# Optimization experiments

Measured on AMD Instinct MI355X. Metric: run time of the kernel, lower is better.

## Reference

```python
import jax, jax.numpy as jnp
import numpy as np

BETA = 0.95
NUM_STEPS = 32


def setup_inputs() -> dict:
    key = jax.random.key(0)
    ks = jax.random.split(key, 6)
    B, IN, D, P = 1024, 512, 256, 8
    total = D * P
    x = jax.random.normal(ks[0], (B, IN), jnp.float32)
    W_proj = jax.random.normal(ks[1], (IN, total), jnp.float32) / np.sqrt(IN)
    b_proj = jnp.zeros((total,), jnp.float32)
    # uniform threshold distribution, sorted: linspace(0.5, 2.0, P)
    thresholds = jnp.linspace(0.5, 2.0, P, dtype=jnp.float32)
    rate_W = jax.random.normal(ks[2], (P, 1), jnp.float32) / np.sqrt(P)
    rate_b = jnp.zeros((1,), jnp.float32)
    conv1_w = jax.random.normal(ks[3], (P // 2, P, 3), jnp.float32) / np.sqrt(P * 3)
    conv1_b = jnp.zeros((P // 2,), jnp.float32)
    conv2_w = jax.random.normal(ks[4], (1, P // 2, 1), jnp.float32) / np.sqrt(P // 2)
    conv2_b = jnp.zeros((1,), jnp.float32)
    fusion = jnp.array([0.6, 0.4], jnp.float32)
    return dict(x=x, W_proj=W_proj, b_proj=b_proj, thresholds=thresholds,
                rate_W=rate_W, rate_b=rate_b, conv1_w=conv1_w, conv1_b=conv1_b,
                conv2_w=conv2_w, conv2_b=conv2_b, fusion=fusion)


def _conv1d(x, w, b):
    # x: [N, C_in, T], w: [C_out, C_in, K] -> [N, C_out, T] (SAME padding)
    y = jax.lax.conv_general_dilated(x, w, window_strides=(1,), padding='SAME',
                                     dimension_numbers=('NCH', 'OIH', 'NCH'))
    return y + b[None, :, None]


def reference(x, W_proj, b_proj, thresholds, rate_W, rate_b,
              conv1_w, conv1_b, conv2_w, conv2_b, fusion):
    B = x.shape[0]
    P = thresholds.shape[0]
    D = W_proj.shape[1] // P
    # constant input current per neuron: [B, D, P]
    I = (x @ W_proj + b_proj).reshape(B, D, P)

    # LIF recurrence (snntorch Leaky, reset_mechanism='subtract'):
    #   reset = H(mem_prev - thr); mem = beta*mem_prev + I - reset*thr; spk = H(mem - thr)
    def step(mem, _):
        reset = (mem > thresholds).astype(mem.dtype)
        mem = BETA * mem + I - reset * thresholds
        spk = (mem > thresholds).astype(mem.dtype)
        return mem, spk

    mem0 = jnp.zeros((B, D, P), x.dtype)
    _, spikes = jax.lax.scan(step, mem0, None, length=NUM_STEPS)  # [T, B, D, P]

    # rate branch
    rates = spikes.mean(axis=0)                        # [B, D, P]
    rate_dec = (rates @ rate_W)[..., 0] + rate_b[0]    # [B, D]

    # temporal branch: [B*D, P, T]
    s = jnp.transpose(spikes, (1, 2, 3, 0)).reshape(B * D, P, NUM_STEPS)
    h = jax.nn.relu(_conv1d(s, conv1_w, conv1_b))
    h = _conv1d(h, conv2_w, conv2_b)                   # [B*D, 1, T]
    temp_dec = h.mean(axis=-1).reshape(B, D)

    fw = jax.nn.softmax(fusion)
    return fw[0] * rate_dec + fw[1] * temp_dec
```

## Files before the change

kernel.cpp:

```cpp
#include <hip/hip_runtime.h>


constexpr int IN_DIM  = 512;
constexpr int D_DIM   = 256;
constexpr int NTOT    = 2048;
constexpr int T_STEPS = 32;

typedef _Float16 f16x8 __attribute__((ext_vector_type(8)));
typedef float    f32x4 __attribute__((ext_vector_type(4)));
typedef ushort   ushort8 __attribute__((ext_vector_type(8)));

#define GLOBAL_AS __attribute__((address_space(1)))
#define LDS_AS    __attribute__((address_space(3)))

__device__ __forceinline__ void split_f16(float v, ushort& h, ushort& l) {
    const _Float16 hf = (_Float16)v;
    const _Float16 lf = (_Float16)((v - (float)hf) * 2048.0f);
    h = __builtin_bit_cast(ushort, hf);
    l = __builtin_bit_cast(ushort, lf);
}

__global__ __launch_bounds__(256)
void popcode_prep(const float* __restrict__ x, const float* __restrict__ Wp,
                  ushort* __restrict__ Ah, ushort* __restrict__ Al,
                  ushort* __restrict__ Bh, ushort* __restrict__ Bl)
{
    __shared__ float tile[64][69];
    const int t = threadIdx.x;
    if (blockIdx.x < 256) {
        const int idx = (blockIdx.x * 256 + t) * 8;
        float v[8];
        *reinterpret_cast<float4*>(v)     = *reinterpret_cast<const float4*>(x + idx);
        *reinterpret_cast<float4*>(v + 4) = *reinterpret_cast<const float4*>(x + idx + 4);
        __align__(16) ushort h[8], l[8];
#pragma unroll
        for (int j = 0; j < 8; ++j) split_f16(v[j], h[j], l[j]);
        *reinterpret_cast<ushort8*>(Ah + idx) = *reinterpret_cast<const ushort8*>(h);
        *reinterpret_cast<ushort8*>(Al + idx) = *reinterpret_cast<const ushort8*>(l);
    } else {
        const int ib = blockIdx.x - 256;
        const int k0 = (ib >> 5) * 64;
        const int c0 = (ib & 31) * 64;
        {
            const int r = t >> 2, cq = (t & 3) * 16;
#pragma unroll
            for (int j = 0; j < 4; ++j)
                *reinterpret_cast<float4*>(&tile[r][cq + j * 4]) =
                    *reinterpret_cast<const float4*>(Wp + (size_t)(k0 + r) * NTOT + c0 + cq + j * 4);
        }
        __syncthreads();
        const int rr = t >> 2, kc2 = (t & 3) * 16;
        __align__(16) ushort h[16], l[16];
#pragma unroll
        for (int j = 0; j < 16; ++j) split_f16(tile[kc2 + j][rr], h[j], l[j]);
        ushort* dh = Bh + (size_t)(c0 + rr) * 512 + k0 + kc2;
        ushort* dl = Bl + (size_t)(c0 + rr) * 512 + k0 + kc2;
        *reinterpret_cast<ushort8*>(dh)     = *reinterpret_cast<const ushort8*>(h);
        *reinterpret_cast<ushort8*>(dh + 8) = *reinterpret_cast<const ushort8*>(h + 8);
        *reinterpret_cast<ushort8*>(dl)     = *reinterpret_cast<const ushort8*>(l);
        *reinterpret_cast<ushort8*>(dl + 8) = *reinterpret_cast<const ushort8*>(l + 8);
    }
}

__global__ __launch_bounds__(256, 2)
void popcode_fused(const ushort* __restrict__ Ah_g, const ushort* __restrict__ Al_g,
                   const ushort* __restrict__ Bh_g, const ushort* __restrict__ Bl_g,
                   const float* __restrict__ bp,
                   const float* __restrict__ thrs,
                   const float* __restrict__ rateW,
                   const float* __restrict__ rateB,
                   const float* __restrict__ c1w,
                   const float* __restrict__ c1b,
                   const float* __restrict__ c2w,
                   const float* __restrict__ c2b,
                   const float* __restrict__ fus,
                   float* __restrict__ out)
{
    __shared__ __align__(16) ushort Lds[2][4][64][32];
    __shared__ float Itile[64][65];
    __shared__ float lut[3][2][16][4];
    __shared__ float wlds[96];

    const int tid  = threadIdx.x;
    const int w    = tid >> 6;
    const int lane = tid & 63;

    const int wg = (blockIdx.x & 7) * 64 + (blockIdx.x >> 3);
    const int b0 = (wg & 15) * 64;
    const int c0 = (wg >> 4) * 64;

    const ushort* gbase = (w == 0) ? Ah_g : (w == 1) ? Al_g : (w == 2) ? Bh_g : Bl_g;
    const int     t0    = (w < 2) ? b0 : c0;
    const int     srow  = lane >> 2;
    const int     schk  = (lane & 3) * 8;

    const int wr = (w >> 1) * 32;
    const int wc = (w & 1) * 32;
    const int lr = lane & 15;
    const int lg = lane >> 4;

    const f32x4 zero = {0.f, 0.f, 0.f, 0.f};
    f32x4 acch[2][2] = {{zero, zero}, {zero, zero}};
    f32x4 accl[2][2] = {{zero, zero}, {zero, zero}};

    LDS_AS char* lds0 = (LDS_AS char*)&Lds[0][0][0][0];

    auto stage = [&](int buf, int kt) {
        const int koff = kt * 32 + schk;
#pragma unroll
        for (int i = 0; i < 4; ++i) {
            const ushort* src = gbase + (size_t)(t0 + srow + 16 * i) * 512 + koff;
            const int loff = __builtin_amdgcn_readfirstlane(buf * 16384 + w * 4096 + i * 1024);
            __builtin_amdgcn_global_load_lds((const GLOBAL_AS uint*)src,
                                             (LDS_AS uint*)(lds0 + loff), 16, 0, 0);
        }
    };

    auto compute = [&](int buf) {
        f16x8 ah[2], al[2], bh[2], bl[2];
#pragma unroll
        for (int m = 0; m < 2; ++m) {
            const int row = wr + m * 16 + lr;
            ah[m] = *(const f16x8*)&Lds[buf][0][row][lg * 8];
            al[m] = *(const f16x8*)&Lds[buf][1][row][lg * 8];
        }
#pragma unroll
        for (int n = 0; n < 2; ++n) {
            const int col = wc + n * 16 + lr;
            bh[n] = *(const f16x8*)&Lds[buf][2][col][lg * 8];
            bl[n] = *(const f16x8*)&Lds[buf][3][col][lg * 8];
        }
#pragma unroll
        for (int m = 0; m < 2; ++m)
#pragma unroll
            for (int n = 0; n < 2; ++n) {
                acch[m][n] = __builtin_amdgcn_mfma_f32_16x16x32_f16(ah[m], bh[n], acch[m][n], 0, 0, 0);
                accl[m][n] = __builtin_amdgcn_mfma_f32_16x16x32_f16(al[m], bh[n], accl[m][n], 0, 0, 0);
                accl[m][n] = __builtin_amdgcn_mfma_f32_16x16x32_f16(ah[m], bl[n], accl[m][n], 0, 0, 0);
            }
    };

    if (tid < 96) wlds[tid] = c1w[tid];
    stage(0, 0);
    __syncthreads();

    for (int e = tid; e < 384; e += 256) {
        const int k  = e >> 7;
        const int j  = (e >> 6) & 1;
        const int nb = (e >> 2) & 15;
        const int c  = e & 3;
        float v = (k == 1 && j == 0) ? c1b[c] : 0.f;
#pragma unroll
        for (int p = 0; p < 4; ++p)
            v = fmaf((float)((nb >> p) & 1), wlds[(c * 8 + j * 4 + p) * 3 + k], v);
        (&lut[0][0][0][0])[e] = v;
    }

    for (int kt = 0; kt < 16; ++kt) {
        if (kt < 15) stage((kt + 1) & 1, kt + 1);
        compute(kt & 1);
        __syncthreads();
    }

    const float s = 1.0f / 2048.0f;
#pragma unroll
    for (int m = 0; m < 2; ++m)
#pragma unroll
        for (int n = 0; n < 2; ++n)
#pragma unroll
            for (int v = 0; v < 4; ++v)
                Itile[wr + m * 16 + lg * 4 + v][wc + n * 16 + lr] =
                    acch[m][n][v] + accl[m][n][v] * s;
    __syncthreads();

    float w2c[4];
#pragma unroll
    for (int c = 0; c < 4; ++c) w2c[c] = c2w[c];
    float rW[8], thrv[8];
#pragma unroll
    for (int p = 0; p < 8; ++p) { rW[p] = rateW[p]; thrv[p] = thrs[p]; }
    const float rb_ = rateB[0];
    const float bb2 = c2b[0];
    const float f0 = fus[0], f1 = fus[1];
    const float fm = fmaxf(f0, f1);
    const float e0 = __expf(f0 - fm), e1 = __expf(f1 - fm);
    const float inv = 1.f / (e0 + e1);
    const float fw0 = e0 * inv, fw1 = e1 * inv;

    const float* lutf = &lut[0][0][0][0];

    for (int half = 0; half < 2; ++half) {
        const int nb   = tid + half * 256;
        const int row  = nb >> 3;
        const int dloc = nb & 7;
        const int dg   = (c0 >> 3) + dloc;

        const float* ip = &Itile[row][dloc * 8];
        const float4 bv0 = *reinterpret_cast<const float4*>(bp + dg * 8);
        const float4 bv1 = *reinterpret_cast<const float4*>(bp + dg * 8 + 4);
        const float bpx[8] = {bv0.x, bv0.y, bv0.z, bv0.w, bv1.x, bv1.y, bv1.z, bv1.w};

        float Iv[8], Imt[8], mem[8];
        bool  spk[8];
#pragma unroll
        for (int p = 0; p < 8; ++p) {
            Iv[p]  = ip[p] + bpx[p];
            Imt[p] = Iv[p] - thrv[p];
            mem[p] = 0.f;
            spk[p] = false;
        }

        unsigned nibL[4] = {0u, 0u, 0u, 0u}, nibH[4] = {0u, 0u, 0u, 0u};
#pragma unroll
        for (int t = 0; t < T_STEPS; ++t) {
            unsigned bl_ = 0u, bh_ = 0u;
#pragma unroll
            for (int p = 0; p < 8; ++p) {
                mem[p] = 0.95f * mem[p] + (spk[p] ? Imt[p] : Iv[p]);
                spk[p] = mem[p] > thrv[p];
            }
#pragma unroll
            for (int p = 0; p < 4; ++p) bl_ |= spk[p] ? (1u << p) : 0u;
#pragma unroll
            for (int p = 4; p < 8; ++p) bh_ |= spk[p] ? (1u << (p - 4)) : 0u;
            nibL[t >> 3] |= bl_ << (4 * (t & 7));
            nibH[t >> 3] |= bh_ << (4 * (t & 7));
        }

        float rsum = 0.f;
#pragma unroll
        for (int p = 0; p < 4; ++p) {
            const unsigned m = 0x11111111u << p;
            const int cL = __popc(nibL[0] & m) + __popc(nibL[1] & m)
                         + __popc(nibL[2] & m) + __popc(nibL[3] & m);
            const int cH = __popc(nibH[0] & m) + __popc(nibH[1] & m)
                         + __popc(nibH[2] & m) + __popc(nibH[3] & m);
            rsum = fmaf((float)cL, rW[p], rsum);
            rsum = fmaf((float)cH, rW[4 + p], rsum);
        }

        auto getn = [](const unsigned* a, int t) -> unsigned {
            return (a[t >> 3] >> (4 * (t & 7))) & 15u;
        };
        float tacc = 0.f;
        unsigned nlp = 0u, nhp = 0u;
        unsigned nlc = getn(nibL, 0), nhc = getn(nibH, 0);
#pragma unroll
        for (int t = 0; t < T_STEPS; ++t) {
            const unsigned nln = (t < 31) ? getn(nibL, t + 1) : 0u;
            const unsigned nhn = (t < 31) ? getn(nibH, t + 1) : 0u;
            const float4 a0 = *reinterpret_cast<const float4*>(lutf + (nlp     ) * 4);
            const float4 a1 = *reinterpret_cast<const float4*>(lutf + (nhp + 16) * 4);
            const float4 b0 = *reinterpret_cast<const float4*>(lutf + (nlc + 32) * 4);
            const float4 b1 = *reinterpret_cast<const float4*>(lutf + (nhc + 48) * 4);
            const float4 c0v = *reinterpret_cast<const float4*>(lutf + (nln + 64) * 4);
            const float4 c1v = *reinterpret_cast<const float4*>(lutf + (nhn + 80) * 4);
            const float h0_ = ((a0.x + a1.x) + (b0.x + b1.x)) + (c0v.x + c1v.x);
            const float h1_ = ((a0.y + a1.y) + (b0.y + b1.y)) + (c0v.y + c1v.y);
            const float h2_ = ((a0.z + a1.z) + (b0.z + b1.z)) + (c0v.z + c1v.z);
            const float h3_ = ((a0.w + a1.w) + (b0.w + b1.w)) + (c0v.w + c1v.w);
            tacc = fmaf(fmaxf(h0_, 0.f), w2c[0], tacc);
            tacc = fmaf(fmaxf(h1_, 0.f), w2c[1], tacc);
            tacc = fmaf(fmaxf(h2_, 0.f), w2c[2], tacc);
            tacc = fmaf(fmaxf(h3_, 0.f), w2c[3], tacc);
            nlp = nlc; nhp = nhc; nlc = nln; nhc = nhn;
        }

        const float rdec = rsum * (1.f / 32.f) + rb_;
        const float temp = tacc * (1.f / 32.f) + bb2;
        out[(b0 + row) * D_DIM + dg] = fw0 * rdec + fw1 * temp;
    }
}

extern "C" void kernel_launch(void* const* d_in, const int* in_sizes, int n_in,
                              void* d_out, int out_size, void* d_ws, size_t ws_size,
                              hipStream_t stream) {
    const float* x     = (const float*)d_in[0];
    const float* Wp    = (const float*)d_in[1];
    const float* bp    = (const float*)d_in[2];
    const float* thrs  = (const float*)d_in[3];
    const float* rateW = (const float*)d_in[4];
    const float* rateB = (const float*)d_in[5];
    const float* c1w   = (const float*)d_in[6];
    const float* c1b   = (const float*)d_in[7];
    const float* c2w   = (const float*)d_in[8];
    const float* c2b   = (const float*)d_in[9];
    const float* fus   = (const float*)d_in[10];
    float* out = (float*)d_out;
    float* ws  = (float*)d_ws;

    ushort* Ah = reinterpret_cast<ushort*>(ws);
    ushort* Al = Ah + 1024 * 512;
    ushort* Bh = Al + 1024 * 512;
    ushort* Bl = Bh + 2048 * 512;

    popcode_prep<<<dim3(512), dim3(256), 0, stream>>>(x, Wp, Ah, Al, Bh, Bl);
    popcode_fused<<<dim3(512), dim3(256), 0, stream>>>(
        Ah, Al, Bh, Bl, bp, thrs, rateW, rateB, c1w, c1b, c2w, c2b, fus, out);
}
```

Baseline: 106.3 us.

## Merge prep and fused kernels into one cooperative launch with grid sync

Replaces the two back-to-back launches (fp16 split/transpose prep, then fused GEMM+LIF) with a single cooperative kernel. The blocks first do the conversion work, then synchronise across the grid before running the fused body. This removes one launch and the gap between kernels, at the cost of a grid-wide barrier. If the cooperative launch fails, it falls back to the original two launches. The prep block mapping is swapped: in the coop kernel, blocks below 256 handle W and the rest handle x, with the W tile reusing the Lds buffer.

Result: slower. 247.4 us (+132.6%).

```diff
diff --git a/kernel.cpp b/kernel.cpp
--- a/kernel.cpp
+++ b/kernel.cpp
@@ -1,4 +1,7 @@
 #include <hip/hip_runtime.h>
+#include <hip/hip_cooperative_groups.h>
+
+namespace cg = cooperative_groups;
 
 
 constexpr int IN_DIM  = 512;
@@ -20,67 +23,65 @@
     l = __builtin_bit_cast(ushort, lf);
 }
 
-__global__ __launch_bounds__(256)
-void popcode_prep(const float* __restrict__ x, const float* __restrict__ Wp,
-                  ushort* __restrict__ Ah, ushort* __restrict__ Al,
-                  ushort* __restrict__ Bh, ushort* __restrict__ Bl)
-{
-    __shared__ float tile[64][69];
-    const int t = threadIdx.x;
-    if (blockIdx.x < 256) {
-        const int idx = (blockIdx.x * 256 + t) * 8;
-        float v[8];
-        *reinterpret_cast<float4*>(v)     = *reinterpret_cast<const float4*>(x + idx);
-        *reinterpret_cast<float4*>(v + 4) = *reinterpret_cast<const float4*>(x + idx + 4);
-        __align__(16) ushort h[8], l[8];
-#pragma unroll
-        for (int j = 0; j < 8; ++j) split_f16(v[j], h[j], l[j]);
-        *reinterpret_cast<ushort8*>(Ah + idx) = *reinterpret_cast<const ushort8*>(h);
-        *reinterpret_cast<ushort8*>(Al + idx) = *reinterpret_cast<const ushort8*>(l);
-    } else {
-        const int ib = blockIdx.x - 256;
-        const int k0 = (ib >> 5) * 64;
-        const int c0 = (ib & 31) * 64;
-        {
-            const int r = t >> 2, cq = (t & 3) * 16;
-#pragma unroll
-            for (int j = 0; j < 4; ++j)
-                *reinterpret_cast<float4*>(&tile[r][cq + j * 4]) =
-                    *reinterpret_cast<const float4*>(Wp + (size_t)(k0 + r) * NTOT + c0 + cq + j * 4);
-        }
-        __syncthreads();
-        const int rr = t >> 2, kc2 = (t & 3) * 16;
-        __align__(16) ushort h[16], l[16];
-#pragma unroll
-        for (int j = 0; j < 16; ++j) split_f16(tile[kc2 + j][rr], h[j], l[j]);
-        ushort* dh = Bh + (size_t)(c0 + rr) * 512 + k0 + kc2;
-        ushort* dl = Bl + (size_t)(c0 + rr) * 512 + k0 + kc2;
-        *reinterpret_cast<ushort8*>(dh)     = *reinterpret_cast<const ushort8*>(h);
-        *reinterpret_cast<ushort8*>(dh + 8) = *reinterpret_cast<const ushort8*>(h + 8);
-        *reinterpret_cast<ushort8*>(dl)     = *reinterpret_cast<const ushort8*>(l);
-        *reinterpret_cast<ushort8*>(dl + 8) = *reinterpret_cast<const ushort8*>(l + 8);
-    }
-}
-
-__global__ __launch_bounds__(256, 2)
-void popcode_fused(const ushort* __restrict__ Ah_g, const ushort* __restrict__ Al_g,
-                   const ushort* __restrict__ Bh_g, const ushort* __restrict__ Bl_g,
-                   const float* __restrict__ bp,
-                   const float* __restrict__ thrs,
-                   const float* __restrict__ rateW,
-                   const float* __restrict__ rateB,
-                   const float* __restrict__ c1w,
-                   const float* __restrict__ c1b,
-                   const float* __restrict__ c2w,
-                   const float* __restrict__ c2b,
-                   const float* __restrict__ fus,
-                   float* __restrict__ out)
-{
-    __shared__ __align__(16) ushort Lds[2][4][64][32];
-    __shared__ float Itile[64][65];
-    __shared__ float lut[3][2][16][4];
-    __shared__ float wlds[96];
-
+__device__ __forceinline__ void conv_x_body(const float* __restrict__ x,
+                                            ushort* __restrict__ Ah,
+                                            ushort* __restrict__ Al,
+                                            int blk, int t)
+{
+    const int idx = (blk * 256 + t) * 8;
+    float v[8];
+    *reinterpret_cast<float4*>(v)     = *reinterpret_cast<const float4*>(x + idx);
+    *reinterpret_cast<float4*>(v + 4) = *reinterpret_cast<const float4*>(x + idx + 4);
+    __align__(16) ushort h[8], l[8];
+#pragma unroll
+    for (int j = 0; j < 8; ++j) split_f16(v[j], h[j], l[j]);
+    *reinterpret_cast<ushort8*>(Ah + idx) = *reinterpret_cast<const ushort8*>(h);
+    *reinterpret_cast<ushort8*>(Al + idx) = *reinterpret_cast<const ushort8*>(l);
+}
+
+__device__ __forceinline__ void conv_w_body(const float* __restrict__ Wp,
+                                            ushort* __restrict__ Bh,
+                                            ushort* __restrict__ Bl,
+                                            float (*tile)[69],
+                                            int ib, int t)
+{
+    const int k0 = (ib >> 5) * 64;
+    const int c0 = (ib & 31) * 64;
+    {
+        const int r = t >> 2, cq = (t & 3) * 16;
+#pragma unroll
+        for (int j = 0; j < 4; ++j)
+            *reinterpret_cast<float4*>(&tile[r][cq + j * 4]) =
+                *reinterpret_cast<const float4*>(Wp + (size_t)(k0 + r) * NTOT + c0 + cq + j * 4);
+    }
+    __syncthreads();
+    const int rr = t >> 2, kc2 = (t & 3) * 16;
+    __align__(16) ushort h[16], l[16];
+#pragma unroll
+    for (int j = 0; j < 16; ++j) split_f16(tile[kc2 + j][rr], h[j], l[j]);
+    ushort* dh = Bh + (size_t)(c0 + rr) * 512 + k0 + kc2;
+    ushort* dl = Bl + (size_t)(c0 + rr) * 512 + k0 + kc2;
+    *reinterpret_cast<ushort8*>(dh)     = *reinterpret_cast<const ushort8*>(h);
+    *reinterpret_cast<ushort8*>(dh + 8) = *reinterpret_cast<const ushort8*>(h + 8);
+    *reinterpret_cast<ushort8*>(dl)     = *reinterpret_cast<const ushort8*>(l);
+    *reinterpret_cast<ushort8*>(dl + 8) = *reinterpret_cast<const ushort8*>(l + 8);
+}
+
+template <typename SyncNone>
+__device__ __forceinline__ void fused_body(
+    const ushort* __restrict__ Ah_g, const ushort* __restrict__ Al_g,
+    const ushort* __restrict__ Bh_g, const ushort* __restrict__ Bl_g,
+    const float* __restrict__ bp, const float* __restrict__ thrs,
+    const float* __restrict__ rateW, const float* __restrict__ rateB,
+    const float* __restrict__ c1w, const float* __restrict__ c1b,
+    const float* __restrict__ c2w, const float* __restrict__ c2b,
+    const float* __restrict__ fus, float* __restrict__ out,
+    ushort (*Lds)[4][64][32],
+    float (*Itile)[65],
+    float* lutf,
+    float* wlds,
+    SyncNone)
+{
     const int tid  = threadIdx.x;
     const int w    = tid >> 6;
     const int lane = tid & 63;
@@ -153,7 +154,7 @@
 #pragma unroll
         for (int p = 0; p < 4; ++p)
             v = fmaf((float)((nb >> p) & 1), wlds[(c * 8 + j * 4 + p) * 3 + k], v);
-        (&lut[0][0][0][0])[e] = v;
+        lutf[e] = v;
     }
 
     for (int kt = 0; kt < 16; ++kt) {
@@ -186,8 +187,6 @@
     const float e0 = __expf(f0 - fm), e1 = __expf(f1 - fm);
     const float inv = 1.f / (e0 + e1);
     const float fw0 = e0 * inv, fw1 = e1 * inv;
-
-    const float* lutf = &lut[0][0][0][0];
 
     for (int half = 0; half < 2; ++half) {
         const int nb   = tid + half * 256;
@@ -272,6 +271,65 @@
     }
 }
 
+__global__ __launch_bounds__(256, 2)
+void popcode_coop(const float* __restrict__ x, const float* __restrict__ Wp,
+                  const float* __restrict__ bp, const float* __restrict__ thrs,
+                  const float* __restrict__ rateW, const float* __restrict__ rateB,
+                  const float* __restrict__ c1w, const float* __restrict__ c1b,
+                  const float* __restrict__ c2w, const float* __restrict__ c2b,
+                  const float* __restrict__ fus, float* __restrict__ out,
+                  ushort* __restrict__ Ah, ushort* __restrict__ Al,
+                  ushort* __restrict__ Bh, ushort* __restrict__ Bl)
+{
+    __shared__ __align__(16) ushort Lds[2][4][64][32];
+    __shared__ float Itile[64][65];
+    __shared__ float lut[384];
+    __shared__ float wlds[96];
+
+    const int tid = threadIdx.x;
+
+    if (blockIdx.x < 256) {
+        float (*tile)[69] = reinterpret_cast<float(*)[69]>(&Lds[0][0][0][0]);
+        conv_w_body(Wp, Bh, Bl, tile, blockIdx.x, tid);
+    } else {
+        conv_x_body(x, Ah, Al, blockIdx.x - 256, tid);
+    }
+
+    __threadfence();
+    cg::this_grid().sync();
+
+    fused_body(Ah, Al, Bh, Bl, bp, thrs, rateW, rateB, c1w, c1b, c2w, c2b,
+               fus, out, Lds, Itile, lut, wlds, 0);
+}
+
+__global__ __launch_bounds__(256)
+void popcode_prep(const float* __restrict__ x, const float* __restrict__ Wp,
+                  ushort* __restrict__ Ah, ushort* __restrict__ Al,
+                  ushort* __restrict__ Bh, ushort* __restrict__ Bl)
+{
+    __shared__ float tile[64][69];
+    const int t = threadIdx.x;
+    if (blockIdx.x < 256) conv_x_body(x, Ah, Al, blockIdx.x, t);
+    else                  conv_w_body(Wp, Bh, Bl, tile, blockIdx.x - 256, t);
+}
+
+__global__ __launch_bounds__(256, 2)
+void popcode_fused(const ushort* __restrict__ Ah_g, const ushort* __restrict__ Al_g,
+                   const ushort* __restrict__ Bh_g, const ushort* __restrict__ Bl_g,
+                   const float* __restrict__ bp, const float* __restrict__ thrs,
+                   const float* __restrict__ rateW, const float* __restrict__ rateB,
+                   const float* __restrict__ c1w, const float* __restrict__ c1b,
+                   const float* __restrict__ c2w, const float* __restrict__ c2b,
+                   const float* __restrict__ fus, float* __restrict__ out)
+{
+    __shared__ __align__(16) ushort Lds[2][4][64][32];
+    __shared__ float Itile[64][65];
+    __shared__ float lut[384];
+    __shared__ float wlds[96];
+    fused_body(Ah_g, Al_g, Bh_g, Bl_g, bp, thrs, rateW, rateB, c1w, c1b,
+               c2w, c2b, fus, out, Lds, Itile, lut, wlds, 0);
+}
+
 extern "C" void kernel_launch(void* const* d_in, const int* in_sizes, int n_in,
                               void* d_out, int out_size, void* d_ws, size_t ws_size,
                               hipStream_t stream) {
@@ -294,7 +352,17 @@
     ushort* Bh = Al + 1024 * 512;
     ushort* Bl = Bh + 2048 * 512;
 
-    popcode_prep<<<dim3(512), dim3(256), 0, stream>>>(x, Wp, Ah, Al, Bh, Bl);
-    popcode_fused<<<dim3(512), dim3(256), 0, stream>>>(
-        Ah, Al, Bh, Bl, bp, thrs, rateW, rateB, c1w, c1b, c2w, c2b, fus, out);
-}
+    void* args[] = { (void*)&x, (void*)&Wp, (void*)&bp, (void*)&thrs,
+                     (void*)&rateW, (void*)&rateB, (void*)&c1w, (void*)&c1b,
+                     (void*)&c2w, (void*)&c2b, (void*)&fus, (void*)&out,
+                     (void*)&Ah, (void*)&Al, (void*)&Bh, (void*)&Bl };
+    const hipError_t err = hipLaunchCooperativeKernel(
+        reinterpret_cast<const void*>(&popcode_coop),
+        dim3(512), dim3(256), args, 0, stream);
+
+    if (err != hipSuccess) {
+        popcode_prep<<<dim3(512), dim3(256), 0, stream>>>(x, Wp, Ah, Al, Bh, Bl);
+        popcode_fused<<<dim3(512), dim3(256), 0, stream>>>(
+            Ah, Al, Bh, Bl, bp, thrs, rateW, rateB, c1w, c1b, c2w, c2b, fus, out);
+    }
+}
```

## Halve fused-kernel column tile, double grid, use byte-indexed conv LUT

Applied to the files above, without the earlier changes.

The fused GEMM+LIF kernel now covers 64x32 output tiles instead of 64x64 and launches 1024 blocks with occupancy hint 4. Each thread handles one neuron group instead of two, which removes the serial half loop. The conv LUT is rebuilt over full 8-bit spike patterns (3x256 entries), so each timestep needs 3 LDS lookups instead of 6. LDS is carved from one aliased buffer, with the LUT built after the GEMM over the staging space. The cost is less reuse of the A tiles, which are loaded twice as often, plus a larger LUT build per block.

New measurement: 145.4 us. 36.8% more time.

```diff
diff --git a/kernel.cpp b/kernel.cpp
--- a/kernel.cpp
+++ b/kernel.cpp
@@ -1,7 +1,6 @@
 #include <hip/hip_runtime.h>
 
 
-constexpr int IN_DIM  = 512;
 constexpr int D_DIM   = 256;
 constexpr int NTOT    = 2048;
 constexpr int T_STEPS = 32;
@@ -20,6 +19,50 @@
     l = __builtin_bit_cast(ushort, lf);
 }
 
+__device__ __forceinline__ void conv_x_body(const float* __restrict__ x,
+                                            ushort* __restrict__ Ah,
+                                            ushort* __restrict__ Al,
+                                            int blk, int t)
+{
+    const int idx = (blk * 256 + t) * 8;
+    float v[8];
+    *reinterpret_cast<float4*>(v)     = *reinterpret_cast<const float4*>(x + idx);
+    *reinterpret_cast<float4*>(v + 4) = *reinterpret_cast<const float4*>(x + idx + 4);
+    __align__(16) ushort h[8], l[8];
+#pragma unroll
+    for (int j = 0; j < 8; ++j) split_f16(v[j], h[j], l[j]);
+    *reinterpret_cast<ushort8*>(Ah + idx) = *reinterpret_cast<const ushort8*>(h);
+    *reinterpret_cast<ushort8*>(Al + idx) = *reinterpret_cast<const ushort8*>(l);
+}
+
+__device__ __forceinline__ void conv_w_body(const float* __restrict__ Wp,
+                                            ushort* __restrict__ Bh,
+                                            ushort* __restrict__ Bl,
+                                            float (*tile)[69],
+                                            int ib, int t)
+{
+    const int k0 = (ib >> 5) * 64;
+    const int c0 = (ib & 31) * 64;
+    {
+        const int r = t >> 2, cq = (t & 3) * 16;
+#pragma unroll
+        for (int j = 0; j < 4; ++j)
+            *reinterpret_cast<float4*>(&tile[r][cq + j * 4]) =
+                *reinterpret_cast<const float4*>(Wp + (size_t)(k0 + r) * NTOT + c0 + cq + j * 4);
+    }
+    __syncthreads();
+    const int rr = t >> 2, kc2 = (t & 3) * 16;
+    __align__(16) ushort h[16], l[16];
+#pragma unroll
+    for (int j = 0; j < 16; ++j) split_f16(tile[kc2 + j][rr], h[j], l[j]);
+    ushort* dh = Bh + (size_t)(c0 + rr) * 512 + k0 + kc2;
+    ushort* dl = Bl + (size_t)(c0 + rr) * 512 + k0 + kc2;
+    *reinterpret_cast<ushort8*>(dh)     = *reinterpret_cast<const ushort8*>(h);
+    *reinterpret_cast<ushort8*>(dh + 8) = *reinterpret_cast<const ushort8*>(h + 8);
+    *reinterpret_cast<ushort8*>(dl)     = *reinterpret_cast<const ushort8*>(l);
+    *reinterpret_cast<ushort8*>(dl + 8) = *reinterpret_cast<const ushort8*>(l + 8);
+}
+
 __global__ __launch_bounds__(256)
 void popcode_prep(const float* __restrict__ x, const float* __restrict__ Wp,
                   ushort* __restrict__ Ah, ushort* __restrict__ Al,
@@ -27,134 +70,93 @@
 {
     __shared__ float tile[64][69];
     const int t = threadIdx.x;
-    if (blockIdx.x < 256) {
-        const int idx = (blockIdx.x * 256 + t) * 8;
-        float v[8];
-        *reinterpret_cast<float4*>(v)     = *reinterpret_cast<const float4*>(x + idx);
-        *reinterpret_cast<float4*>(v + 4) = *reinterpret_cast<const float4*>(x + idx + 4);
-        __align__(16) ushort h[8], l[8];
-#pragma unroll
-        for (int j = 0; j < 8; ++j) split_f16(v[j], h[j], l[j]);
-        *reinterpret_cast<ushort8*>(Ah + idx) = *reinterpret_cast<const ushort8*>(h);
-        *reinterpret_cast<ushort8*>(Al + idx) = *reinterpret_cast<const ushort8*>(l);
-    } else {
-        const int ib = blockIdx.x - 256;
-        const int k0 = (ib >> 5) * 64;
-        const int c0 = (ib & 31) * 64;
-        {
-            const int r = t >> 2, cq = (t & 3) * 16;
-#pragma unroll
-            for (int j = 0; j < 4; ++j)
-                *reinterpret_cast<float4*>(&tile[r][cq + j * 4]) =
-                    *reinterpret_cast<const float4*>(Wp + (size_t)(k0 + r) * NTOT + c0 + cq + j * 4);
-        }
-        __syncthreads();
-        const int rr = t >> 2, kc2 = (t & 3) * 16;
-        __align__(16) ushort h[16], l[16];
-#pragma unroll
-        for (int j = 0; j < 16; ++j) split_f16(tile[kc2 + j][rr], h[j], l[j]);
-        ushort* dh = Bh + (size_t)(c0 + rr) * 512 + k0 + kc2;
-        ushort* dl = Bl + (size_t)(c0 + rr) * 512 + k0 + kc2;
-        *reinterpret_cast<ushort8*>(dh)     = *reinterpret_cast<const ushort8*>(h);
-        *reinterpret_cast<ushort8*>(dh + 8) = *reinterpret_cast<const ushort8*>(h + 8);
-        *reinterpret_cast<ushort8*>(dl)     = *reinterpret_cast<const ushort8*>(l);
-        *reinterpret_cast<ushort8*>(dl + 8) = *reinterpret_cast<const ushort8*>(l + 8);
-    }
-}
-
-__global__ __launch_bounds__(256, 2)
+    if (blockIdx.x < 256) conv_x_body(x, Ah, Al, blockIdx.x, t);
+    else                  conv_w_body(Wp, Bh, Bl, tile, blockIdx.x - 256, t);
+}
+
+__global__ __launch_bounds__(256, 4)
 void popcode_fused(const ushort* __restrict__ Ah_g, const ushort* __restrict__ Al_g,
                    const ushort* __restrict__ Bh_g, const ushort* __restrict__ Bl_g,
-                   const float* __restrict__ bp,
-                   const float* __restrict__ thrs,
-                   const float* __restrict__ rateW,
-                   const float* __restrict__ rateB,
-                   const float* __restrict__ c1w,
-                   const float* __restrict__ c1b,
-                   const float* __restrict__ c2w,
-                   const float* __restrict__ c2b,
-                   const float* __restrict__ fus,
-                   float* __restrict__ out)
-{
-    __shared__ __align__(16) ushort Lds[2][4][64][32];
-    __shared__ float Itile[64][65];
-    __shared__ float lut[3][2][16][4];
-    __shared__ float wlds[96];
+                   const float* __restrict__ bp, const float* __restrict__ thrs,
+                   const float* __restrict__ rateW, const float* __restrict__ rateB,
+                   const float* __restrict__ c1w, const float* __restrict__ c1b,
+                   const float* __restrict__ c2w, const float* __restrict__ c2b,
+                   const float* __restrict__ fus, float* __restrict__ out)
+{
+    __shared__ __align__(16) char smem[33664];
+    LDS_AS char* lds0 = (LDS_AS char*)smem;
 
     const int tid  = threadIdx.x;
     const int w    = tid >> 6;
     const int lane = tid & 63;
 
-    const int wg = (blockIdx.x & 7) * 64 + (blockIdx.x >> 3);
+    const int wg = ((blockIdx.x & 7) << 7) | (blockIdx.x >> 3);
     const int b0 = (wg & 15) * 64;
-    const int c0 = (wg >> 4) * 64;
+    const int c0 = (wg >> 4) * 32;
 
     const ushort* gbase = (w == 0) ? Ah_g : (w == 1) ? Al_g : (w == 2) ? Bh_g : Bl_g;
     const int     t0    = (w < 2) ? b0 : c0;
     const int     srow  = lane >> 2;
     const int     schk  = (lane & 3) * 8;
+    const int     poff  = (w < 2) ? (w * 4096) : (8192 + (w - 2) * 2048);
 
     const int wr = (w >> 1) * 32;
-    const int wc = (w & 1) * 32;
+    const int wc = (w & 1) * 16;
     const int lr = lane & 15;
     const int lg = lane >> 4;
 
     const f32x4 zero = {0.f, 0.f, 0.f, 0.f};
-    f32x4 acch[2][2] = {{zero, zero}, {zero, zero}};
-    f32x4 accl[2][2] = {{zero, zero}, {zero, zero}};
-
-    LDS_AS char* lds0 = (LDS_AS char*)&Lds[0][0][0][0];
+    f32x4 acch[2] = {zero, zero};
+    f32x4 accl[2] = {zero, zero};
 
     auto stage = [&](int buf, int kt) {
         const int koff = kt * 32 + schk;
-#pragma unroll
-        for (int i = 0; i < 4; ++i) {
-            const ushort* src = gbase + (size_t)(t0 + srow + 16 * i) * 512 + koff;
-            const int loff = __builtin_amdgcn_readfirstlane(buf * 16384 + w * 4096 + i * 1024);
-            __builtin_amdgcn_global_load_lds((const GLOBAL_AS uint*)src,
-                                             (LDS_AS uint*)(lds0 + loff), 16, 0, 0);
+        const int base = buf * 12288 + poff;
+        if (w < 2) {
+#pragma unroll
+            for (int i = 0; i < 4; ++i) {
+                const ushort* src = gbase + (size_t)(t0 + srow + 16 * i) * 512 + koff;
+                const int loff = __builtin_amdgcn_readfirstlane(base + i * 1024);
+                __builtin_amdgcn_global_load_lds((const GLOBAL_AS uint*)src,
+                                                 (LDS_AS uint*)(lds0 + loff), 16, 0, 0);
+            }
+        } else {
+#pragma unroll
+            for (int i = 0; i < 2; ++i) {
+                const ushort* src = gbase + (size_t)(t0 + srow + 16 * i) * 512 + koff;
+                const int loff = __builtin_amdgcn_readfirstlane(base + i * 1024);
+                __builtin_amdgcn_global_load_lds((const GLOBAL_AS uint*)src,
+                                                 (LDS_AS uint*)(lds0 + loff), 16, 0, 0);
+            }
         }
     };
 
     auto compute = [&](int buf) {
-        f16x8 ah[2], al[2], bh[2], bl[2];
+        const int rbase = buf * 12288;
+        f16x8 ah[2], al[2], bh, bl;
 #pragma unroll
         for (int m = 0; m < 2; ++m) {
             const int row = wr + m * 16 + lr;
-            ah[m] = *(const f16x8*)&Lds[buf][0][row][lg * 8];
-            al[m] = *(const f16x8*)&Lds[buf][1][row][lg * 8];
-        }
-#pragma unroll
-        for (int n = 0; n < 2; ++n) {
-            const int col = wc + n * 16 + lr;
-            bh[n] = *(const f16x8*)&Lds[buf][2][col][lg * 8];
-            bl[n] = *(const f16x8*)&Lds[buf][3][col][lg * 8];
-        }
-#pragma unroll
-        for (int m = 0; m < 2; ++m)
-#pragma unroll
-            for (int n = 0; n < 2; ++n) {
-                acch[m][n] = __builtin_amdgcn_mfma_f32_16x16x32_f16(ah[m], bh[n], acch[m][n], 0, 0, 0);
-                accl[m][n] = __builtin_amdgcn_mfma_f32_16x16x32_f16(al[m], bh[n], accl[m][n], 0, 0, 0);
-                accl[m][n] = __builtin_amdgcn_mfma_f32_16x16x32_f16(ah[m], bl[n], accl[m][n], 0, 0, 0);
-            }
+            ah[m] = *reinterpret_cast<const f16x8*>(smem + rbase +        row * 64 + lg * 16);
+            al[m] = *reinterpret_cast<const f16x8*>(smem + rbase + 4096 + row * 64 + lg * 16);
+        }
+        {
+            const int col = wc + lr;
+            bh = *reinterpret_cast<const f16x8*>(smem + rbase +  8192 + col * 64 + lg * 16);
+            bl = *reinterpret_cast<const f16x8*>(smem + rbase + 10240 + col * 64 + lg * 16);
+        }
+#pragma unroll
+        for (int m = 0; m < 2; ++m) {
+            acch[m] = __builtin_amdgcn_mfma_f32_16x16x32_f16(ah[m], bh, acch[m], 0, 0, 0);
+            accl[m] = __builtin_amdgcn_mfma_f32_16x16x32_f16(al[m], bh, accl[m], 0, 0, 0);
+            accl[m] = __builtin_amdgcn_mfma_f32_16x16x32_f16(ah[m], bl, accl[m], 0, 0, 0);
+        }
     };
 
+    float* wlds = (float*)(smem + 33280);
     if (tid < 96) wlds[tid] = c1w[tid];
     stage(0, 0);
     __syncthreads();
-
-    for (int e = tid; e < 384; e += 256) {
-        const int k  = e >> 7;
-        const int j  = (e >> 6) & 1;
-        const int nb = (e >> 2) & 15;
-        const int c  = e & 3;
-        float v = (k == 1 && j == 0) ? c1b[c] : 0.f;
-#pragma unroll
-        for (int p = 0; p < 4; ++p)
-            v = fmaf((float)((nb >> p) & 1), wlds[(c * 8 + j * 4 + p) * 3 + k], v);
-        (&lut[0][0][0][0])[e] = v;
-    }
 
     for (int kt = 0; kt < 16; ++kt) {
         if (kt < 15) stage((kt + 1) & 1, kt + 1);
@@ -162,15 +164,26 @@
         __syncthreads();
     }
 
+    float* lutf = (float*)smem;
+    for (int e = tid; e < 3072; e += 256) {
+        const int k    = e >> 10;
+        const int byte = (e >> 2) & 255;
+        const int c    = e & 3;
+        float v = (k == 1) ? c1b[c] : 0.f;
+#pragma unroll
+        for (int p = 0; p < 8; ++p)
+            v = fmaf((float)((byte >> p) & 1), wlds[(c * 8 + p) * 3 + k], v);
+        lutf[e] = v;
+    }
+
+    float* it = (float*)(smem + 24576);
     const float s = 1.0f / 2048.0f;
 #pragma unroll
     for (int m = 0; m < 2; ++m)
 #pragma unroll
-        for (int n = 0; n < 2; ++n)
-#pragma unroll
-            for (int v = 0; v < 4; ++v)
-                Itile[wr + m * 16 + lg * 4 + v][wc + n * 16 + lr] =
-                    acch[m][n][v] + accl[m][n][v] * s;
+        for (int v = 0; v < 4; ++v)
+            it[(wr + m * 16 + lg * 4 + v) * 34 + wc + lr] =
+                acch[m][v] + accl[m][v] * s;
     __syncthreads();
 
     float w2c[4];
@@ -187,89 +200,75 @@
     const float inv = 1.f / (e0 + e1);
     const float fw0 = e0 * inv, fw1 = e1 * inv;
 
-    const float* lutf = &lut[0][0][0][0];
-
-    for (int half = 0; half < 2; ++half) {
-        const int nb   = tid + half * 256;
-        const int row  = nb >> 3;
-        const int dloc = nb & 7;
-        const int dg   = (c0 >> 3) + dloc;
-
-        const float* ip = &Itile[row][dloc * 8];
-        const float4 bv0 = *reinterpret_cast<const float4*>(bp + dg * 8);
-        const float4 bv1 = *reinterpret_cast<const float4*>(bp + dg * 8 + 4);
-        const float bpx[8] = {bv0.x, bv0.y, bv0.z, bv0.w, bv1.x, bv1.y, bv1.z, bv1.w};
-
-        float Iv[8], Imt[8], mem[8];
-        bool  spk[8];
+    const int row  = tid >> 2;
+    const int dloc = tid & 3;
+    const int dg   = (c0 >> 3) + dloc;
+
+    const float* ip  = it + row * 34 + dloc * 8;
+    const float4 bv0 = *reinterpret_cast<const float4*>(bp + dg * 8);
+    const float4 bv1 = *reinterpret_cast<const float4*>(bp + dg * 8 + 4);
+    const float bpx[8] = {bv0.x, bv0.y, bv0.z, bv0.w, bv1.x, bv1.y, bv1.z, bv1.w};
+
+    float Iv[8], Imt[8], mem[8];
+    bool  spk[8];
+#pragma unroll
+    for (int p = 0; p < 8; ++p) {
+        Iv[p]  = ip[p] + bpx[p];
+        Imt[p] = Iv[p] - thrv[p];
+        mem[p] = 0.f;
+        spk[p] = false;
+    }
+
+    unsigned wrd[8] = {0u, 0u, 0u, 0u, 0u, 0u, 0u, 0u};
+#pragma unroll
+    for (int t = 0; t < T_STEPS; ++t) {
+        unsigned by = 0u;
 #pragma unroll
         for (int p = 0; p < 8; ++p) {
-            Iv[p]  = ip[p] + bpx[p];
-            Imt[p] = Iv[p] - thrv[p];
-            mem[p] = 0.f;
-            spk[p] = false;
-        }
-
-        unsigned nibL[4] = {0u, 0u, 0u, 0u}, nibH[4] = {0u, 0u, 0u, 0u};
-#pragma unroll
-        for (int t = 0; t < T_STEPS; ++t) {
-            unsigned bl_ = 0u, bh_ = 0u;
-#pragma unroll
-            for (int p = 0; p < 8; ++p) {
-                mem[p] = 0.95f * mem[p] + (spk[p] ? Imt[p] : Iv[p]);
-                spk[p] = mem[p] > thrv[p];
-            }
-#pragma unroll
-            for (int p = 0; p < 4; ++p) bl_ |= spk[p] ? (1u << p) : 0u;
-#pragma unroll
-            for (int p = 4; p < 8; ++p) bh_ |= spk[p] ? (1u << (p - 4)) : 0u;
-            nibL[t >> 3] |= bl_ << (4 * (t & 7));
-            nibH[t >> 3] |= bh_ << (4 * (t & 7));
-        }
-
-        float rsum = 0.f;
-#pragma unroll
-        for (int p = 0; p < 4; ++p) {
-            const unsigned m = 0x11111111u << p;
-            const int cL = __popc(nibL[0] & m) + __popc(nibL[1] & m)
-                         + __popc(nibL[2] & m) + __popc(nibL[3] & m);
-            const int cH = __popc(nibH[0] & m) + __popc(nibH[1] & m)
-                         + __popc(nibH[2] & m) + __popc(nibH[3] & m);
-            rsum = fmaf((float)cL, rW[p], rsum);
-            rsum = fmaf((float)cH, rW[4 + p], rsum);
-        }
-
-        auto getn = [](const unsigned* a, int t) -> unsigned {
-            return (a[t >> 3] >> (4 * (t & 7))) & 15u;
-        };
-        float tacc = 0.f;
-        unsigned nlp = 0u, nhp = 0u;
-        unsigned nlc = getn(nibL, 0), nhc = getn(nibH, 0);
-#pragma unroll
-        for (int t = 0; t < T_STEPS; ++t) {
-            const unsigned nln = (t < 31) ? getn(nibL, t + 1) : 0u;
-            const unsigned nhn = (t < 31) ? getn(nibH, t + 1) : 0u;
-            const float4 a0 = *reinterpret_cast<const float4*>(lutf + (nlp     ) * 4);
-            const float4 a1 = *reinterpret_cast<const float4*>(lutf + (nhp + 16) * 4);
-            const float4 b0 = *reinterpret_cast<const float4*>(lutf + (nlc + 32) * 4);
-            const float4 b1 = *reinterpret_cast<const float4*>(lutf + (nhc + 48) * 4);
-            const float4 c0v = *reinterpret_cast<const float4*>(lutf + (nln + 64) * 4);
-            const float4 c1v = *reinterpret_cast<const float4*>(lutf + (nhn + 80) * 4);
-            const float h0_ = ((a0.x + a1.x) + (b0.x + b1.x)) + (c0v.x + c1v.x);
-            const float h1_ = ((a0.y + a1.y) + (b0.y + b1.y)) + (c0v.y + c1v.y);
-            const float h2_ = ((a0.z + a1.z) + (b0.z + b1.z)) + (c0v.z + c1v.z);
-            const float h3_ = ((a0.w + a1.w) + (b0.w + b1.w)) + (c0v.w + c1v.w);
-            tacc = fmaf(fmaxf(h0_, 0.f), w2c[0], tacc);
-            tacc = fmaf(fmaxf(h1_, 0.f), w2c[1], tacc);
-            tacc = fmaf(fmaxf(h2_, 0.f), w2c[2], tacc);
-            tacc = fmaf(fmaxf(h3_, 0.f), w2c[3], tacc);
-            nlp = nlc; nhp = nhc; nlc = nln; nhc = nhn;
-        }
-
-        const float rdec = rsum * (1.f / 32.f) + rb_;
-        const float temp = tacc * (1.f / 32.f) + bb2;
-        out[(b0 + row) * D_DIM + dg] = fw0 * rdec + fw1 * temp;
-    }
+            mem[p] = 0.95f * mem[p] + (spk[p] ? Imt[p] : Iv[p]);
+            spk[p] = mem[p] > thrv[p];
+            by |= spk[p] ? (1u << p) : 0u;
+        }
+        wrd[t >> 2] |= by << (8 * (t & 3));
+    }
+
+    float rsum = 0.f;
+#pragma unroll
+    for (int p = 0; p < 8; ++p) {
+        const unsigned m = 0x01010101u << p;
+        int cnt = 0;
+#pragma unroll
+        for (int q = 0; q < 8; ++q) cnt += __popc(wrd[q] & m);
+        rsum = fmaf((float)cnt, rW[p], rsum);
+    }
+
+    auto getb = [&](int t) -> unsigned {
+        return (wrd[t >> 2] >> (8 * (t & 3))) & 255u;
+    };
+    float tacc = 0.f;
+    unsigned bprev = 0u;
+    unsigned bcur  = getb(0);
+#pragma unroll
+    for (int t = 0; t < T_STEPS; ++t) {
+        const unsigned bnext = (t < 31) ? getb(t + 1) : 0u;
+        const float4 fa = *reinterpret_cast<const float4*>(lutf + bprev * 4);
+        const float4 fb = *reinterpret_cast<const float4*>(lutf + 1024 + bcur * 4);
+        const float4 fc = *reinterpret_cast<const float4*>(lutf + 2048 + bnext * 4);
+        const float h0_ = (fa.x + fb.x) + fc.x;
+        const float h1_ = (fa.y + fb.y) + fc.y;
+        const float h2_ = (fa.z + fb.z) + fc.z;
+        const float h3_ = (fa.w + fb.w) + fc.w;
+        tacc = fmaf(fmaxf(h0_, 0.f), w2c[0], tacc);
+        tacc = fmaf(fmaxf(h1_, 0.f), w2c[1], tacc);
+        tacc = fmaf(fmaxf(h2_, 0.f), w2c[2], tacc);
+        tacc = fmaf(fmaxf(h3_, 0.f), w2c[3], tacc);
+        bprev = bcur;
+        bcur  = bnext;
+    }
+
+    const float rdec = rsum * (1.f / 32.f) + rb_;
+    const float temp = tacc * (1.f / 32.f) + bb2;
+    out[(b0 + row) * D_DIM + dg] = fw0 * rdec + fw1 * temp;
 }
 
 extern "C" void kernel_launch(void* const* d_in, const int* in_sizes, int n_in,
@@ -295,6 +294,6 @@
     ushort* Bl = Bh + 2048 * 512;
 
     popcode_prep<<<dim3(512), dim3(256), 0, stream>>>(x, Wp, Ah, Al, Bh, Bl);
-    popcode_fused<<<dim3(512), dim3(256), 0, stream>>>(
+    popcode_fused<<<dim3(1024), dim3(256), 0, stream>>>(
         Ah, Al, Bh, Bl, bp, thrs, rateW, rateB, c1w, c1b, c2w, c2b, fus, out);
 }
```
